# Kernel tuning notes

Hardware: AMD Instinct MI355X
Metric: run time of the kernel (lower is better)

## Reference

```python
import jax, jax.numpy as jnp
import numpy as np

B, T, D = 4, 4096, 768      # batch, tokens, n_embd
S = 1024                    # memory_slots (divides T -> adaptive pool == window mean)
K = 8                       # memory_topk
RW = 0.1                    # memory_retrieval_weight


def setup_inputs() -> dict:
    key = jax.random.key(0)
    ks = jax.random.split(key, 10)
    w = 1.0 / np.sqrt(D).astype(np.float32)
    return {
        "x": jax.random.normal(ks[0], (B, T, D), jnp.float32),
        "Wq": jax.random.normal(ks[1], (D, D), jnp.float32) * w,
        "bq": jnp.zeros((D,), jnp.float32),
        "Wk": jax.random.normal(ks[2], (D, D), jnp.float32) * w,
        "bk": jnp.zeros((D,), jnp.float32),
        "Wv": jax.random.normal(ks[3], (D, D), jnp.float32) * w,
        "bv": jnp.zeros((D,), jnp.float32),
        "Wp": jax.random.normal(ks[4], (D, D), jnp.float32) * w,
        "bp": jnp.zeros((D,), jnp.float32),
        "persistent_memory": jax.random.normal(ks[5], (S, D), jnp.float32),
    }


def reference(x, Wq, bq, Wk, bk, Wv, bv, Wp, bp, persistent_memory):
    # _build_memory_slots: adaptive_avg_pool1d to S slots; T % S == 0 so it is a window mean
    pooled = x.reshape(B, S, T // S, D).mean(axis=2)                    # [B,S,D]
    pers = jnp.broadcast_to(persistent_memory[None], (B, S, D))         # persistent bank
    slots = jnp.concatenate([pooled, pers], axis=1)                     # [B,2S,D]

    q = x @ Wq + bq                                                     # [B,T,D]
    k = slots @ Wk + bk                                                 # [B,2S,D]
    v = slots @ Wv + bv                                                 # [B,2S,D]

    scores = jnp.einsum('btd,bsd->bts', q, k) / jnp.sqrt(jnp.float32(D))  # [B,T,2S]
    top_s, top_i = jax.lax.top_k(scores, K)                             # [B,T,K]
    w = jax.nn.softmax(top_s, axis=-1)                                  # softmax over top-k only

    # gather top-k values: [B,T,K,D]
    vg = jnp.take_along_axis(v, top_i.reshape(B, T * K)[:, :, None], axis=1)
    vg = vg.reshape(B, T, K, D)
    retrieved = jnp.einsum('btk,btkd->btd', w, vg)                      # weighted combine

    return RW * (retrieved @ Wp + bp)                                   # proj * retrieval_weight
```

## Files before the change

### kernel.cpp

```cpp
#include <hip/hip_runtime.h>
#include <math.h>

#define BB 4
#define TT 4096
#define DD 768
#define SS 1024
#define S2 2048
#define KTOP 8
#define RWEIGHT 0.1f
#define TAU 2e-4f
#define AMB_CAP 256

typedef __attribute__((ext_vector_type(8))) _Float16 f16x8;
typedef __attribute__((ext_vector_type(4))) float f32x4;
typedef _Float16 f16;

__device__ __forceinline__ size_t fragoff(int row, int k) {
    return ((size_t)(row >> 4) * 24 + (k >> 5)) * 512 +
           (((row & 15) + (((k >> 3) & 3) << 4)) << 3) + (k & 7);
}

__global__ __launch_bounds__(256) void build_pooled_all(
    const float* __restrict__ x, float* __restrict__ slots)
{
    int i = blockIdx.x * 256 + threadIdx.x;
    int s2 = i / DD;
    int d = i - s2 * DD;
    int b = s2 >> 10, s = s2 & 1023;
    const float* xb = x + (size_t)b * TT * DD + (size_t)(4 * s) * DD + d;
    slots[i] = 0.25f * (xb[0] + xb[DD] + xb[2 * DD] + xb[3 * DD]);
}

__global__ __launch_bounds__(256) void transpose_split(
    const float* __restrict__ W0, const float* __restrict__ W1,
    const float* __restrict__ W2, const float* __restrict__ W3,
    f16* __restrict__ WQh, f16* __restrict__ WQm,
    f16* __restrict__ WKh, f16* __restrict__ WKm,
    f16* __restrict__ WVh, f16* __restrict__ WPh,
    float* __restrict__ WkT32)
{
    const int z = blockIdx.z;
    const float* W = (z == 0) ? W0 : (z == 1) ? W1 : (z == 2) ? W2 : W3;
    __shared__ float t[32][33];
    int bx = blockIdx.x * 32, by = blockIdx.y * 32;
    int lx = threadIdx.x & 31, ly = threadIdx.x >> 5;
#pragma unroll
    for (int r = 0; r < 32; r += 8)
        t[ly + r][lx] = W[(size_t)(bx + ly + r) * 768 + by + lx];
    __syncthreads();
#pragma unroll
    for (int r = 0; r < 32; r += 8) {
        float w = t[lx][ly + r];
        int n = by + ly + r, k = bx + lx;
        size_t fo = fragoff(n, k);
        f16 h = (f16)w;
        if (z == 0) { WQh[fo] = h; WQm[fo] = (f16)(w - (float)h); }
        else if (z == 1) { WKh[fo] = h; WKm[fo] = (f16)(w - (float)h);
                           WkT32[(size_t)n * 768 + k] = w; }
        else if (z == 2) { WVh[fo] = h; }
        else { WPh[fo] = h; }
    }
}

__global__ void zeroN(int* p) { p[threadIdx.x] = 0; }

__device__ __forceinline__ void tile_split_prod(
    const float* __restrict__ A, int arow0,
    const f16* __restrict__ BhF, const f16* __restrict__ BmF, int bncol,
    const float* __restrict__ bias,
    f16* __restrict__ ChF, f16* __restrict__ CmF, int crow0,
    f16* LAh, f16* LAm)
{
    const int tid = threadIdx.x;
    const int lane = tid & 63;
    const int wc = (tid >> 6) & 1;
    const int wr = (tid >> 7) & 1;
    const int srow = tid >> 1, c0 = tid & 1;
    const int p0 = c0 ^ (srow & 3) ^ ((srow >> 2) & 1);
    const int wo0 = srow * 32 + p0 * 8, wo1 = wo0 ^ 16;
    const int csw = (((lane >> 4) ^ (lane & 3) ^ ((lane >> 2) & 1)) * 8);

    f32x4 acc[4][4];
#pragma unroll
    for (int i = 0; i < 4; ++i)
#pragma unroll
        for (int j = 0; j < 4; ++j) acc[i][j] = (f32x4){0.f, 0.f, 0.f, 0.f};

    const float* pa = A + (size_t)(arow0 + srow) * 768 + c0 * 8;
    const int rbB0 = bncol / 16 + wc * 4;

    float4 a0 = *(const float4*)(pa);
    float4 a1 = *(const float4*)(pa + 4);
    float4 a2 = *(const float4*)(pa + 16);
    float4 a3 = *(const float4*)(pa + 20);

    for (int kb = 0; kb < 24; ++kb) {
        __syncthreads();
        {
            float av[16] = {a0.x, a0.y, a0.z, a0.w, a1.x, a1.y, a1.z, a1.w,
                            a2.x, a2.y, a2.z, a2.w, a3.x, a3.y, a3.z, a3.w};
            f16x8 h, m;
#pragma unroll
            for (int j = 0; j < 8; ++j) {
                f16 hh = (f16)av[j]; h[j] = hh; m[j] = (f16)(av[j] - (float)hh);
            }
            *(f16x8*)&LAh[wo0] = h; *(f16x8*)&LAm[wo0] = m;
#pragma unroll
            for (int j = 0; j < 8; ++j) {
                f16 hh = (f16)av[j + 8]; h[j] = hh; m[j] = (f16)(av[j + 8] - (float)hh);
            }
            *(f16x8*)&LAh[wo1] = h; *(f16x8*)&LAm[wo1] = m;
        }
        __syncthreads();

        if (kb + 1 < 24) {
            int k0 = (kb + 1) * 32;
            a0 = *(const float4*)(pa + k0);
            a1 = *(const float4*)(pa + k0 + 4);
            a2 = *(const float4*)(pa + k0 + 16);
            a3 = *(const float4*)(pa + k0 + 20);
        }

        f16x8 fbh[4], fbm[4];
#pragma unroll
        for (int ni = 0; ni < 4; ++ni) {
            size_t off = ((size_t)(rbB0 + ni) * 24 + kb) * 512 + lane * 8;
            fbh[ni] = *(const f16x8*)&BhF[off];
            fbm[ni] = *(const f16x8*)&BmF[off];
        }
        f16x8 fah[4], fam[4];
#pragma unroll
        for (int mi = 0; mi < 4; ++mi) {
            int off = (wr * 64 + mi * 16 + (lane & 15)) * 32 + csw;
            fah[mi] = *(const f16x8*)&LAh[off];
            fam[mi] = *(const f16x8*)&LAm[off];
        }
#pragma unroll
        for (int mi = 0; mi < 4; ++mi)
#pragma unroll
            for (int ni = 0; ni < 4; ++ni) {
                acc[mi][ni] = __builtin_amdgcn_mfma_f32_16x16x32_f16(
                    fah[mi], fbh[ni], acc[mi][ni], 0, 0, 0);
                acc[mi][ni] = __builtin_amdgcn_mfma_f32_16x16x32_f16(
                    fah[mi], fbm[ni], acc[mi][ni], 0, 0, 0);
                acc[mi][ni] = __builtin_amdgcn_mfma_f32_16x16x32_f16(
                    fam[mi], fbh[ni], acc[mi][ni], 0, 0, 0);
            }
    }

    const int orow0 = wr * 64 + (lane >> 4) * 4;
    const int ocol0 = wc * 64 + (lane & 15);
#pragma unroll
    for (int mi = 0; mi < 4; ++mi)
#pragma unroll
        for (int ni = 0; ni < 4; ++ni) {
            int kk = bncol + ocol0 + ni * 16;
            float badd = bias[kk];
            int rbase = crow0 + orow0 + mi * 16;
#pragma unroll
            for (int r = 0; r < 4; ++r) {
                float val = acc[mi][ni][r] + badd;
                f16 h = (f16)val;
                size_t fo = fragoff(rbase + r, kk);
                ChF[fo] = h;
                CmF[fo] = (f16)(val - (float)h);
            }
        }
}

__device__ __forceinline__ void tile_1p_prod(
    const float* __restrict__ A, int arow0,
    const f16* __restrict__ BhF, int bncol,
    const float* __restrict__ bias,
    f16* __restrict__ Co, int crow0, f16* LA)
{
    const int tid = threadIdx.x;
    const int lane = tid & 63;
    const int wc = (tid >> 6) & 1;
    const int wr = (tid >> 7) & 1;
    const int srow = tid >> 1, c0 = tid & 1;
    const int p0 = c0 ^ (srow & 3) ^ ((srow >> 2) & 1);
    const int wo0 = srow * 32 + p0 * 8, wo1 = wo0 ^ 16;
    const int csw = (((lane >> 4) ^ (lane & 3) ^ ((lane >> 2) & 1)) * 8);

    f32x4 acc[4][4];
#pragma unroll
    for (int i = 0; i < 4; ++i)
#pragma unroll
        for (int j = 0; j < 4; ++j) acc[i][j] = (f32x4){0.f, 0.f, 0.f, 0.f};

    const float* pa = A + (size_t)(arow0 + srow) * 768 + c0 * 8;
    const int rbB0 = bncol / 16 + wc * 4;

    float4 a0 = *(const float4*)(pa);
    float4 a1 = *(const float4*)(pa + 4);
    float4 a2 = *(const float4*)(pa + 16);
    float4 a3 = *(const float4*)(pa + 20);

    for (int kb = 0; kb < 24; ++kb) {
        __syncthreads();
        {
            f16x8 h;
            h[0] = (f16)a0.x; h[1] = (f16)a0.y; h[2] = (f16)a0.z; h[3] = (f16)a0.w;
            h[4] = (f16)a1.x; h[5] = (f16)a1.y; h[6] = (f16)a1.z; h[7] = (f16)a1.w;
            *(f16x8*)&LA[wo0] = h;
            h[0] = (f16)a2.x; h[1] = (f16)a2.y; h[2] = (f16)a2.z; h[3] = (f16)a2.w;
            h[4] = (f16)a3.x; h[5] = (f16)a3.y; h[6] = (f16)a3.z; h[7] = (f16)a3.w;
            *(f16x8*)&LA[wo1] = h;
        }
        __syncthreads();

        if (kb + 1 < 24) {
            int k0 = (kb + 1) * 32;
            a0 = *(const float4*)(pa + k0);
            a1 = *(const float4*)(pa + k0 + 4);
            a2 = *(const float4*)(pa + k0 + 16);
            a3 = *(const float4*)(pa + k0 + 20);
        }

        f16x8 fbh[4];
#pragma unroll
        for (int ni = 0; ni < 4; ++ni)
            fbh[ni] = *(const f16x8*)&BhF[((size_t)(rbB0 + ni) * 24 + kb) * 512 + lane * 8];
        f16x8 fah[4];
#pragma unroll
        for (int mi = 0; mi < 4; ++mi)
            fah[mi] = *(const f16x8*)&LA[(wr * 64 + mi * 16 + (lane & 15)) * 32 + csw];
#pragma unroll
        for (int mi = 0; mi < 4; ++mi)
#pragma unroll
            for (int ni = 0; ni < 4; ++ni)
                acc[mi][ni] = __builtin_amdgcn_mfma_f32_16x16x32_f16(
                    fah[mi], fbh[ni], acc[mi][ni], 0, 0, 0);
    }

    const int orow0 = wr * 64 + (lane >> 4) * 4;
    const int ocol0 = wc * 64 + (lane & 15);
#pragma unroll
    for (int mi = 0; mi < 4; ++mi)
#pragma unroll
        for (int ni = 0; ni < 4; ++ni) {
            size_t col = (size_t)bncol + ocol0 + ni * 16;
            float badd = bias[col];
            size_t rbase = (size_t)crow0 + orow0 + mi * 16;
#pragma unroll
            for (int r = 0; r < 4; ++r)
                Co[(rbase + r) * 768 + col] = (f16)(acc[mi][ni][r] + badd);
        }
}

__device__ __forceinline__ void tile_proj_frag(
    const f16* __restrict__ AF, int arow0,
    const f16* __restrict__ BhF, int bncol,
    const float* __restrict__ bias,
    float* __restrict__ Co, int crow0)
{
    const int tid = threadIdx.x;
    const int lane = tid & 63;
    const int wc = (tid >> 6) & 1;
    const int wr = (tid >> 7) & 1;

    f32x4 acc[4][4];
#pragma unroll
    for (int i = 0; i < 4; ++i)
#pragma unroll
        for (int j = 0; j < 4; ++j) acc[i][j] = (f32x4){0.f, 0.f, 0.f, 0.f};

    const int rbA0 = arow0 / 16 + wr * 4;
    const int rbB0 = bncol / 16 + wc * 4;

    for (int kb = 0; kb < 24; ++kb) {
        f16x8 fah[4], fbh[4];
#pragma unroll
        for (int mi = 0; mi < 4; ++mi)
            fah[mi] = *(const f16x8*)&AF[((size_t)(rbA0 + mi) * 24 + kb) * 512 + lane * 8];
#pragma unroll
        for (int ni = 0; ni < 4; ++ni)
            fbh[ni] = *(const f16x8*)&BhF[((size_t)(rbB0 + ni) * 24 + kb) * 512 + lane * 8];
#pragma unroll
        for (int mi = 0; mi < 4; ++mi)
#pragma unroll
            for (int ni = 0; ni < 4; ++ni)
                acc[mi][ni] = __builtin_amdgcn_mfma_f32_16x16x32_f16(
                    fah[mi], fbh[ni], acc[mi][ni], 0, 0, 0);
    }

    const int orow0 = wr * 64 + (lane >> 4) * 4;
    const int ocol0 = wc * 64 + (lane & 15);
#pragma unroll
    for (int mi = 0; mi < 4; ++mi)
#pragma unroll
        for (int ni = 0; ni < 4; ++ni) {
            size_t col = (size_t)bncol + ocol0 + ni * 16;
            float badd = RWEIGHT * bias[col];
            size_t rbase = (size_t)crow0 + orow0 + mi * 16;
#pragma unroll
            for (int r = 0; r < 4; ++r)
                Co[(rbase + r) * 768 + col] = RWEIGHT * acc[mi][ni][r] + badd;
        }
}

__device__ __forceinline__ void tile_scores_frag(
    const f16* __restrict__ qhF, const f16* __restrict__ qmF, int arow0,
    const f16* __restrict__ khF, const f16* __restrict__ kmF, int bncol,
    float* __restrict__ C, float alpha)
{
    const int tid = threadIdx.x;
    const int lane = tid & 63;
    const int wc = (tid >> 6) & 1;
    const int wr = (tid >> 7) & 1;

    f32x4 acc[4][4];
#pragma unroll
    for (int i = 0; i < 4; ++i)
#pragma unroll
        for (int j = 0; j < 4; ++j) acc[i][j] = (f32x4){0.f, 0.f, 0.f, 0.f};

    const int rbA0 = arow0 / 16 + wr * 4;
    const int rbB0 = bncol / 16 + wc * 4;

    for (int kb = 0; kb < 24; ++kb) {
        f16x8 fah[4], fam[4], fbh[4], fbm[4];
#pragma unroll
        for (int mi = 0; mi < 4; ++mi) {
            size_t off = ((size_t)(rbA0 + mi) * 24 + kb) * 512 + lane * 8;
            fah[mi] = *(const f16x8*)&qhF[off];
            fam[mi] = *(const f16x8*)&qmF[off];
        }
#pragma unroll
        for (int ni = 0; ni < 4; ++ni) {
            size_t off = ((size_t)(rbB0 + ni) * 24 + kb) * 512 + lane * 8;
            fbh[ni] = *(const f16x8*)&khF[off];
            fbm[ni] = *(const f16x8*)&kmF[off];
        }
#pragma unroll
        for (int mi = 0; mi < 4; ++mi)
#pragma unroll
            for (int ni = 0; ni < 4; ++ni) {
                acc[mi][ni] = __builtin_amdgcn_mfma_f32_16x16x32_f16(
                    fah[mi], fbh[ni], acc[mi][ni], 0, 0, 0);
                acc[mi][ni] = __builtin_amdgcn_mfma_f32_16x16x32_f16(
                    fah[mi], fbm[ni], acc[mi][ni], 0, 0, 0);
                acc[mi][ni] = __builtin_amdgcn_mfma_f32_16x16x32_f16(
                    fam[mi], fbh[ni], acc[mi][ni], 0, 0, 0);
            }
    }

    const int orow0 = wr * 64 + (lane >> 4) * 4;
    const int ocol0 = wc * 64 + (lane & 15);
#pragma unroll
    for (int mi = 0; mi < 4; ++mi)
#pragma unroll
        for (int ni = 0; ni < 4; ++ni) {
            size_t col = (size_t)bncol + ocol0 + ni * 16;
            size_t rbase = (size_t)arow0 + orow0 + mi * 16;
#pragma unroll
            for (int r = 0; r < 4; ++r)
                C[(rbase + r) * S2 + col] = alpha * acc[mi][ni][r];
        }
}

__global__ __launch_bounds__(256) void megaSelProd(
    int nSel, const float* __restrict__ scores, const f16* __restrict__ v16r,
    f16* __restrict__ retrW, int gbase,
    int* __restrict__ ambc, int* __restrict__ ambgrow, int* __restrict__ cand,
    float* __restrict__ oldw, f16* __restrict__ vsave,
    int hasQ, int hasKV, int doPm,
    const float* __restrict__ xq, const float* __restrict__ slots_b,
    const float* __restrict__ pm,
    const f16* __restrict__ WQh, const f16* __restrict__ WQm,
    const f16* __restrict__ WKh, const f16* __restrict__ WKm,
    const f16* __restrict__ WVh,
    const float* __restrict__ bq, const float* __restrict__ bk,
    const float* __restrict__ bv,
    f16* __restrict__ qh, f16* __restrict__ qm,
    f16* __restrict__ kh, f16* __restrict__ km,
    f16* __restrict__ v16w, f16* __restrict__ v16w2)
{
    __shared__ f16 LAh[4096], LAm[4096];
    int t = blockIdx.x;

    if (hasQ) {
        if (t < 192) {
            tile_split_prod(xq, (t / 6) * 128, WQh, WQm, (t % 6) * 128, bq,
                            qh, qm, (t / 6) * 128, LAh, LAm);
            return;
        }
        t -= 192;
    }
    if (hasKV) {
        if (t < 48) {
            tile_split_prod(slots_b, (t / 6) * 128, WKh, WKm, (t % 6) * 128, bk,
                            kh, km, (t / 6) * 128, LAh, LAm);
            return;
        }
        t -= 48;
        if (doPm) {
            if (t < 48) {
                tile_split_prod(pm, (t / 6) * 128, WKh, WKm, (t % 6) * 128, bk,
                                kh, km, 1024 + (t / 6) * 128, LAh, LAm);
                return;
            }
            t -= 48;
        }
        if (t < 48) {
            tile_1p_prod(slots_b, (t / 6) * 128, WVh, (t % 6) * 128, bv,
                         v16w, (t / 6) * 128, LAh);
            return;
        }
        t -= 48;
        if (doPm) {
            if (t < 48) {
                tile_1p_prod(pm, (t / 6) * 128, WVh, (t % 6) * 128, bv,
                             v16w, 1024 + (t / 6) * 128, LAh);
                return;
            }
            t -= 48;
            if (t < 48) {
                tile_1p_prod(pm, (t / 6) * 128, WVh, (t % 6) * 128, bv,
                             v16w2, 1024 + (t / 6) * 128, LAh);
                return;
            }
            t -= 48;
        }
    }
    if (t >= nSel) return;

    const int lane = threadIdx.x & 63;
    const int wave = threadIdx.x >> 6;
    const int row = t * 4 + wave;
    const float* srow = scores + (size_t)row * S2;
    float vals[32];
#pragma unroll
    for (int i = 0; i < 32; ++i) vals[i] = srow[lane + (i << 6)];

    float topv[16]; int topi[16];
    bool amb = false;
    int nr = 9;
    for (int r = 0; r < 16; ++r) {
        if (r >= nr) break;
        float bvv = -3.4e38f; int bii = 0x7fffffff;
#pragma unroll
        for (int i = 0; i < 32; ++i)
            if (vals[i] > bvv) { bvv = vals[i]; bii = lane + (i << 6); }
#pragma unroll
        for (int off = 32; off > 0; off >>= 1) {
            float ov = __shfl_xor(bvv, off);
            int   oi = __shfl_xor(bii, off);
            if (ov > bvv || (ov == bvv && oi < bii)) { bvv = ov; bii = oi; }
        }
        topv[r] = bvv; topi[r] = bii;
        if ((bii & 63) == lane) vals[bii >> 6] = -3.4e38f;
        if (r == 8) {
            amb = (topv[7] - topv[8]) < TAU;
            if (amb) nr = 16;
        }
    }

    float m = topv[0], w[KTOP], sum = 0.f;
#pragma unroll
    for (int r = 0; r < KTOP; ++r) { w[r] = expf(topv[r] - m); sum += w[r]; }
    float inv = 1.f / sum;
#pragma unroll
    for (int r = 0; r < KTOP; ++r) w[r] *= inv;

    if (amb) {
        int idx = 0;
        if (lane == 0) idx = atomicAdd(ambc, 1);
        idx = __shfl(idx, 0);
        if (idx < AMB_CAP) {
            if (lane == 0) ambgrow[idx] = gbase + row;
            if (lane < 16) cand[idx * 16 + lane] = topi[lane];
            if (lane < KTOP) oldw[idx * KTOP + lane] = w[lane];
            f16* vs = vsave + (size_t)idx * 16 * 768;
            for (int cc = lane; cc < 16 * 96; cc += 64) {
                int cr = cc / 96, ch = cc - cr * 96;
                *(f16x8*)&vs[(size_t)cr * 768 + ch * 8] =
                    *(const f16x8*)&v16r[(size_t)topi[cr] * 768 + ch * 8];
            }
        }
    }

    for (int c = lane; c < 96; c += 64) {
        float o[8] = {0, 0, 0, 0, 0, 0, 0, 0};
#pragma unroll
        for (int r = 0; r < KTOP; ++r) {
            f16x8 vv = *(const f16x8*)&v16r[(size_t)topi[r] * 768 + c * 8];
#pragma unroll
            for (int j = 0; j < 8; ++j) o[j] += w[r] * (float)vv[j];
        }
        f16x8 hx;
#pragma unroll
        for (int j = 0; j < 8; ++j) hx[j] = (f16)o[j];
        size_t fo = ((size_t)(row >> 4) * 24 + (c >> 2)) * 512 +
                    (((row & 15) + ((c & 3) << 4)) << 3);
        *(f16x8*)&retrW[fo] = hx;
    }
}

__global__ __launch_bounds__(256) void megaScoresProj(
    int nSc, const f16* __restrict__ qh, const f16* __restrict__ qm,
    const f16* __restrict__ kh, const f16* __restrict__ km,
    float* __restrict__ scores, float alpha,
    const f16* __restrict__ retrR, const f16* __restrict__ WPh,
    const float* __restrict__ bp, float* __restrict__ outp)
{
    int t = blockIdx.x;
    if (t < nSc) {
        tile_scores_frag(qh, qm, (t >> 4) * 128, kh, km, (t & 15) * 128,
                         scores, alpha);
        return;
    }
    t -= nSc;
    tile_proj_frag(retrR, (t / 6) * 128, WPh, (t % 6) * 128, bp,
                   outp, (t / 6) * 128);
}

__global__ __launch_bounds__(256) void fixA(
    const int* __restrict__ amb_count, const int* __restrict__ amb_grow,
    const float* __restrict__ x, const float* __restrict__ Wq,
    const float* __restrict__ bq, double* __restrict__ q64buf)
{
    int n = *amb_count; if (n > AMB_CAP) n = AMB_CAP;
    const int i = blockIdx.y;
    if (i >= n) return;
    const int tid = threadIdx.x;
    const int jl = tid & 63;
    const int ks = tid >> 6;
    const int j = blockIdx.x * 64 + jl;
    const int grow = amb_grow[i];

    __shared__ float xs[768];
    __shared__ double ps[4][64];
    for (int t = tid; t < 768; t += 256) xs[t] = x[(size_t)grow * 768 + t];
    __syncthreads();

    double a0 = 0.0, a1 = 0.0;
    const float* wp = Wq + j;
    const int k0 = ks * 192;
#pragma unroll 8
    for (int k = 0; k < 192; k += 2) {
        a0 = fma((double)xs[k0 + k],     (double)wp[(size_t)(k0 + k) * 768],     a0);
        a1 = fma((double)xs[k0 + k + 1], (double)wp[(size_t)(k0 + k + 1) * 768], a1);
    }
    ps[ks][jl] = a0 + a1;
    __syncthreads();
    if (ks == 0)
        q64buf[(size_t)i * 768 + j] =
            ((ps[0][jl] + ps[1][jl]) + (ps[2][jl] + ps[3][jl])) + (double)bq[j];
}

__global__ __launch_bounds__(256) void fixB(
    const int* __restrict__ amb_count,
    const float* __restrict__ WkT, const float* __restrict__ bk,
    const double* __restrict__ q64buf,
    double* __restrict__ ubuf, double* __restrict__ bkqbuf)
{
    int n = *amb_count; if (n > AMB_CAP) n = AMB_CAP;
    const int i = blockIdx.y;
    if (i >= n) return;
    const int tid = threadIdx.x;
    const int tl = tid & 63;
    const int js = tid >> 6;
    const int t = blockIdx.x * 64 + tl;

    __shared__ double qs[768];
    __shared__ double ps[4][64];
    const double* qrow = q64buf + (size_t)i * 768;
    for (int k = tid; k < 768; k += 256) qs[k] = qrow[k];
    __syncthreads();

    double a0 = 0.0, a1 = 0.0;
    const float* wp = WkT + t;
    const int j0 = js * 192;
#pragma unroll 8
    for (int k = 0; k < 192; k += 2) {
        a0 = fma((double)wp[(size_t)(j0 + k) * 768],     qs[j0 + k],     a0);
        a1 = fma((double)wp[(size_t)(j0 + k + 1) * 768], qs[j0 + k + 1], a1);
    }
    ps[js][tl] = a0 + a1;
    __syncthreads();
    if (js == 0)
        ubuf[(size_t)i * 768 + t] = (ps[0][tl] + ps[1][tl]) + (ps[2][tl] + ps[3][tl]);

    if (blockIdx.x == 0 && tid < 64) {
        double p = 0.0;
#pragma unroll
        for (int c = 0; c < 12; ++c) {
            int jj = tid + (c << 6);
            p = fma((double)bk[jj], qs[jj], p);
        }
#pragma unroll
        for (int off = 32; off; off >>= 1) p += __shfl_xor(p, off);
        if (tid == 0) bkqbuf[i] = p;
    }
}

__global__ __launch_bounds__(256) void fixC(
    const int* __restrict__ amb_count, const int* __restrict__ amb_grow,
    const float* __restrict__ x, const float* __restrict__ pm,
    const int* __restrict__ cand, const float* __restrict__ oldw,
    const double* __restrict__ ubuf, const double* __restrict__ bkqbuf,
    const f16* __restrict__ vsave, float* __restrict__ dret)
{
    int n = *amb_count; if (n > AMB_CAP) n = AMB_CAP;
    const int i = blockIdx.x;
    if (i >= n) return;
    const int tid = threadIdx.x;
    const int lane = tid & 63;
    const int wave = tid >> 6;
    const int grow = amb_grow[i];
    const float* xb = x + (size_t)(grow >> 12) * TT * 768;

    __shared__ double us[768];
    __shared__ double cs_s[16];
    __shared__ float coef[16];

    const double* urow = ubuf + (size_t)i * 768;
    for (int t = tid; t < 768; t += 256) us[t] = urow[t];
    __syncthreads();

    const double ISQ = 1.0 / sqrt((double)DD);
    const double bkq = bkqbuf[i];
#pragma unroll
    for (int c = wave; c < 16; c += 4) {
        int s = cand[i * 16 + c];
        double p = 0.0;
        if (s < SS) {
            const float* xr = xb + (size_t)(4 * s) * 768;
#pragma unroll
            for (int t = 0; t < 12; ++t) {
                int j2 = lane + (t << 6);
                double sv = 0.25 * ((double)xr[j2] + (double)xr[j2 + 768] +
                                    (double)xr[j2 + 1536] + (double)xr[j2 + 2304]);
                p = fma(sv, us[j2], p);
            }
        } else {
            const float* pr = pm + (size_t)(s - SS) * 768;
#pragma unroll
            for (int t = 0; t < 12; ++t) {
                int j2 = lane + (t << 6);
                p = fma((double)pr[j2], us[j2], p);
            }
        }
#pragma unroll
        for (int off = 32; off; off >>= 1) p += __shfl_xor(p, off);
        if (lane == 0) cs_s[c] = (p + bkq) * ISQ;
    }
    __syncthreads();

    if (tid == 0) {
        double cs[16]; int ci[16];
        for (int c = 0; c < 16; ++c) { cs[c] = cs_s[c]; ci[c] = cand[i * 16 + c]; }
        unsigned used = 0;
        double sv[KTOP]; int sp[KTOP];
        for (int r = 0; r < KTOP; ++r) {
            int bi = -1;
            for (int c = 0; c < 16; ++c) {
                if (used & (1u << c)) continue;
                if (bi < 0 || cs[c] > cs[bi] ||
                    (cs[c] == cs[bi] && ci[c] < ci[bi])) bi = c;
            }
            used |= (1u << bi); sv[r] = cs[bi]; sp[r] = bi;
        }
        double mx = sv[0], es[KTOP], ssum = 0.0;
        for (int r = 0; r < KTOP; ++r) { es[r] = exp(sv[r] - mx); ssum += es[r]; }
        for (int c = 0; c < 16; ++c) coef[c] = (c < KTOP) ? -oldw[i * KTOP + c] : 0.f;
        for (int r = 0; r < KTOP; ++r) coef[sp[r]] += (float)(es[r] / ssum);
    }
    __syncthreads();

    const f16* vs = vsave + (size_t)i * 16 * 768;
    for (int j = tid; j < 768; j += 256) {
        float d = 0.f;
#pragma unroll
        for (int c = 0; c < 16; ++c) d += coef[c] * (float)vs[(size_t)c * 768 + j];
        dret[(size_t)i * 768 + j] = d;
    }
}

__global__ __launch_bounds__(256) void fixD(
    const int* __restrict__ amb_count, const int* __restrict__ amb_grow,
    const float* __restrict__ dret, const float* __restrict__ Wp,
    float* __restrict__ out)
{
    int n = *amb_count; if (n > AMB_CAP) n = AMB_CAP;
    const int i = blockIdx.y;
    if (i >= n) return;
    const int tid = threadIdx.x;
    const int jl = tid & 63;
    const int ks = tid >> 6;
    const int j = blockIdx.x * 64 + jl;
    const int grow = amb_grow[i];

    __shared__ float ds[768];
    __shared__ float ps[4][64];
    for (int t = tid; t < 768; t += 256) ds[t] = dret[(size_t)i * 768 + t];
    __syncthreads();

    float a0 = 0.f, a1 = 0.f;
    const float* wp = Wp + j;
    const int k0 = ks * 192;
#pragma unroll 8
    for (int k = 0; k < 192; k += 2) {
        a0 = fmaf(ds[k0 + k],     wp[(size_t)(k0 + k) * 768],     a0);
        a1 = fmaf(ds[k0 + k + 1], wp[(size_t)(k0 + k + 1) * 768], a1);
    }
    ps[ks][jl] = a0 + a1;
    __syncthreads();
    if (ks == 0)
        out[(size_t)grow * 768 + j] +=
            RWEIGHT * ((ps[0][jl] + ps[1][jl]) + (ps[2][jl] + ps[3][jl]));
}

extern "C" void kernel_launch(void* const* d_in, const int* in_sizes, int n_in,
                              void* d_out, int out_size, void* d_ws, size_t ws_size,
                              hipStream_t stream)
{
    const float* x  = (const float*)d_in[0];
    const float* Wq = (const float*)d_in[1];
    const float* bq = (const float*)d_in[2];
    const float* Wk = (const float*)d_in[3];
    const float* bk = (const float*)d_in[4];
    const float* Wv = (const float*)d_in[5];
    const float* bv = (const float*)d_in[6];
    const float* Wp = (const float*)d_in[7];
    const float* bp = (const float*)d_in[8];
    const float* pm = (const float*)d_in[9];
    float* out = (float*)d_out;
    float* ws  = (float*)d_ws;

    const float inv_sqrt_d = (float)(1.0 / sqrt((double)DD));
    const size_t TD  = (size_t)TT * DD;
    const size_t SD  = (size_t)SS * DD;
    const size_t WSZ = (size_t)DD * DD;

    float* p = ws;
    f16* WQh = (f16*)p; p += WSZ / 2;
    f16* WQm = (f16*)p; p += WSZ / 2;
    f16* WKh = (f16*)p; p += WSZ / 2;
    f16* WKm = (f16*)p; p += WSZ / 2;
    f16* WVh = (f16*)p; p += WSZ / 2;
    f16* WPh = (f16*)p; p += WSZ / 2;
    float* WkT32 = p; p += WSZ;
    float* slots_all = p; p += (size_t)BB * SD;
    f16* qh = (f16*)p; p += TD / 2;
    f16* qm = (f16*)p; p += TD / 2;
    f16* kh = (f16*)p; p += SD;
    f16* km = (f16*)p; p += SD;
    f16* v16a = (f16*)p; p += SD;
    f16* v16b = (f16*)p; p += SD;
    f16* retrA = (f16*)p; p += TD / 2;
    f16* retrB = (f16*)p; p += TD / 2;
    double* q64buf = (double*)p; p += (size_t)AMB_CAP * DD * 2;
    double* ubuf   = (double*)p; p += (size_t)AMB_CAP * DD * 2;
    double* bkqbuf = (double*)p; p += AMB_CAP * 2;
    int* cand = (int*)p; p += (size_t)AMB_CAP * 16;
    float* oldw = p; p += (size_t)AMB_CAP * KTOP;
    f16* vsave = (f16*)p; p += (size_t)AMB_CAP * 16 * DD / 2;
    float* dret = p; p += (size_t)AMB_CAP * DD;
    int* ambc = (int*)p; p += 64;
    int* ambgrow = (int*)p; p += AMB_CAP;
    float* scores = p;

    transpose_split<<<dim3(24, 24, 4), 256, 0, stream>>>(
        Wq, Wk, Wv, Wp, WQh, WQm, WKh, WKm, WVh, WPh, WkT32);
    zeroN<<<1, 64, 0, stream>>>(ambc);
    build_pooled_all<<<(BB * SS * DD) / 256, 256, 0, stream>>>(x, slots_all);

    megaSelProd<<<432, 256, 0, stream>>>(
        0, nullptr, nullptr, nullptr, 0, ambc, ambgrow, cand, oldw, vsave,
        1, 1, 1, x, slots_all, pm,
        WQh, WQm, WKh, WKm, WVh, bq, bk, bv, qh, qm, kh, km, v16a, v16b);
    megaScoresProj<<<512, 256, 0, stream>>>(
        512, qh, qm, kh, km, scores, inv_sqrt_d, nullptr, WPh, bp, nullptr);

    for (int b = 1; b < BB; ++b) {
        f16* v16w = (b & 1) ? v16b : v16a;
        f16* v16r = ((b - 1) & 1) ? v16b : v16a;
        f16* retrW = ((b - 1) & 1) ? retrB : retrA;

        megaSelProd<<<1312, 256, 0, stream>>>(
            1024, scores, v16r, retrW, (b - 1) * TT,
            ambc, ambgrow, cand, oldw, vsave,
            1, 1, 0, x + (size_t)b * TD, slots_all + (size_t)b * SD, nullptr,
            WQh, WQm, WKh, WKm, WVh, bq, bk, bv, qh, qm, kh, km, v16w, nullptr);
        megaScoresProj<<<704, 256, 0, stream>>>(
            512, qh, qm, kh, km, scores, inv_sqrt_d,
            retrW, WPh, bp, out + (size_t)(b - 1) * TD);
    }

    f16* v16r3 = v16b;
    f16* retrW3 = retrB;
    megaSelProd<<<1024, 256, 0, stream>>>(
        1024, scores, v16r3, retrW3, 3 * TT,
        ambc, ambgrow, cand, oldw, vsave,
        0, 0, 0, nullptr, nullptr, nullptr,
        WQh, WQm, WKh, WKm, WVh, bq, bk, bv, qh, qm, kh, km, nullptr, nullptr);
    megaScoresProj<<<192, 256, 0, stream>>>(
        0, nullptr, nullptr, nullptr, nullptr, nullptr, 0.f,
        retrW3, WPh, bp, out + (size_t)3 * TD);

    fixA<<<dim3(12, AMB_CAP), 256, 0, stream>>>(ambc, ambgrow, x, Wq, bq, q64buf);
    fixB<<<dim3(12, AMB_CAP), 256, 0, stream>>>(ambc, WkT32, bk, q64buf, ubuf, bkqbuf);
    fixC<<<AMB_CAP, 256, 0, stream>>>(ambc, ambgrow, x, pm, cand, oldw,
                                      ubuf, bkqbuf, vsave, dret);
    fixD<<<dim3(12, AMB_CAP), 256, 0, stream>>>(ambc, ambgrow, dret, Wp, out);
}
```

Measured before the change: 663.9 us.

## Store q/k/retrieved as row-major planes and stage through swizzled LDS

Intermediate q, k and retrieved tensors are now written row-major instead of in the pre-swizzled MFMA fragment layout. The scores and projection tiles load them with coalesced global reads into XOR-swizzled shared memory, prefetching the next k-slice into registers. The aim is cheaper, more coalesced epilogue stores in the producers. The cost is extra LDS traffic, two barriers per k-step, and 32 KB of shared memory per block in the scores/proj kernel, which may lower occupancy.

```diff
diff --git a/kernel.cpp b/kernel.cpp
--- a/kernel.cpp
+++ b/kernel.cpp
@@ -68,7 +68,7 @@
     const float* __restrict__ A, int arow0,
     const f16* __restrict__ BhF, const f16* __restrict__ BmF, int bncol,
     const float* __restrict__ bias,
-    f16* __restrict__ ChF, f16* __restrict__ CmF, int crow0,
+    f16* __restrict__ Ch, f16* __restrict__ Cm, int crow0,
     f16* LAh, f16* LAm)
 {
     const int tid = threadIdx.x;
@@ -154,16 +154,16 @@
     for (int mi = 0; mi < 4; ++mi)
 #pragma unroll
         for (int ni = 0; ni < 4; ++ni) {
-            int kk = bncol + ocol0 + ni * 16;
-            float badd = bias[kk];
-            int rbase = crow0 + orow0 + mi * 16;
+            size_t col = (size_t)bncol + ocol0 + ni * 16;
+            float badd = bias[col];
+            size_t rbase = (size_t)crow0 + orow0 + mi * 16;
 #pragma unroll
             for (int r = 0; r < 4; ++r) {
                 float val = acc[mi][ni][r] + badd;
                 f16 h = (f16)val;
-                size_t fo = fragoff(rbase + r, kk);
-                ChF[fo] = h;
-                CmF[fo] = (f16)(val - (float)h);
+                size_t idx = (rbase + r) * 768 + col;
+                Ch[idx] = h;
+                Cm[idx] = (f16)(val - (float)h);
             }
         }
 }
@@ -249,16 +249,20 @@
         }
 }
 
-__device__ __forceinline__ void tile_proj_frag(
-    const f16* __restrict__ AF, int arow0,
+__device__ __forceinline__ void tile_proj(
+    const f16* __restrict__ A, int arow0,
     const f16* __restrict__ BhF, int bncol,
     const float* __restrict__ bias,
-    float* __restrict__ Co, int crow0)
+    float* __restrict__ Co, int crow0, f16* LA)
 {
     const int tid = threadIdx.x;
     const int lane = tid & 63;
     const int wc = (tid >> 6) & 1;
     const int wr = (tid >> 7) & 1;
+    const int srow = tid >> 1, c0 = tid & 1;
+    const int p0 = c0 ^ (srow & 3) ^ ((srow >> 2) & 1);
+    const int wo0 = srow * 32 + p0 * 8, wo1 = wo0 ^ 16;
+    const int csw = (((lane >> 4) ^ (lane & 3) ^ ((lane >> 2) & 1)) * 8);
 
     f32x4 acc[4][4];
 #pragma unroll
@@ -266,17 +270,32 @@
 #pragma unroll
         for (int j = 0; j < 4; ++j) acc[i][j] = (f32x4){0.f, 0.f, 0.f, 0.f};
 
-    const int rbA0 = arow0 / 16 + wr * 4;
+    const f16* pa = A + (size_t)(arow0 + srow) * 768 + c0 * 8;
     const int rbB0 = bncol / 16 + wc * 4;
 
+    f16x8 ah0 = *(const f16x8*)(pa);
+    f16x8 ah1 = *(const f16x8*)(pa + 16);
+
     for (int kb = 0; kb < 24; ++kb) {
-        f16x8 fah[4], fbh[4];
-#pragma unroll
-        for (int mi = 0; mi < 4; ++mi)
-            fah[mi] = *(const f16x8*)&AF[((size_t)(rbA0 + mi) * 24 + kb) * 512 + lane * 8];
+        __syncthreads();
+        *(f16x8*)&LA[wo0] = ah0;
+        *(f16x8*)&LA[wo1] = ah1;
+        __syncthreads();
+
+        if (kb + 1 < 24) {
+            int k0 = (kb + 1) * 32;
+            ah0 = *(const f16x8*)(pa + k0);
+            ah1 = *(const f16x8*)(pa + k0 + 16);
+        }
+
+        f16x8 fbh[4];
 #pragma unroll
         for (int ni = 0; ni < 4; ++ni)
             fbh[ni] = *(const f16x8*)&BhF[((size_t)(rbB0 + ni) * 24 + kb) * 512 + lane * 8];
+        f16x8 fah[4];
+#pragma unroll
+        for (int mi = 0; mi < 4; ++mi)
+            fah[mi] = *(const f16x8*)&LA[(wr * 64 + mi * 16 + (lane & 15)) * 32 + csw];
 #pragma unroll
         for (int mi = 0; mi < 4; ++mi)
 #pragma unroll
@@ -300,15 +319,21 @@
         }
 }
 
-__device__ __forceinline__ void tile_scores_frag(
-    const f16* __restrict__ qhF, const f16* __restrict__ qmF, int arow0,
-    const f16* __restrict__ khF, const f16* __restrict__ kmF, int bncol,
-    float* __restrict__ C, float alpha)
+__device__ __forceinline__ void tile_scores_planes(
+    const f16* __restrict__ qh, const f16* __restrict__ qm, int arow0,
+    const f16* __restrict__ kh, const f16* __restrict__ km, int bncol,
+    float* __restrict__ C, float alpha,
+    f16* LAh, f16* LAm, f16* LBh, f16* LBm)
 {
     const int tid = threadIdx.x;
     const int lane = tid & 63;
     const int wc = (tid >> 6) & 1;
     const int wr = (tid >> 7) & 1;
+    const int srow = tid >> 1, c0 = tid & 1;
+    const int p0 = c0 ^ (srow & 3) ^ ((srow >> 2) & 1);
+    const int wo0 = srow * 32 + p0 * 8, wo1 = wo0 ^ 16;
+    const int csw = (((lane >> 4) ^ (lane & 3) ^ ((lane >> 2) & 1)) * 8);
+    const size_t bn = (size_t)bncol;
 
     f32x4 acc[4][4];
 #pragma unroll
@@ -316,22 +341,51 @@
 #pragma unroll
         for (int j = 0; j < 4; ++j) acc[i][j] = (f32x4){0.f, 0.f, 0.f, 0.f};
 
-    const int rbA0 = arow0 / 16 + wr * 4;
-    const int rbB0 = bncol / 16 + wc * 4;
-
-    for (int kb = 0; kb < 24; ++kb) {
+    const f16* pah = qh + (size_t)(arow0 + srow) * 768 + c0 * 8;
+    const f16* pam = qm + (size_t)(arow0 + srow) * 768 + c0 * 8;
+    const f16* pbh = kh + (bn + srow) * 768 + c0 * 8;
+    const f16* pbm = km + (bn + srow) * 768 + c0 * 8;
+
+    f16x8 ah0 = *(const f16x8*)(pah);
+    f16x8 ah1 = *(const f16x8*)(pah + 16);
+    f16x8 am0 = *(const f16x8*)(pam);
+    f16x8 am1 = *(const f16x8*)(pam + 16);
+    f16x8 bh0 = *(const f16x8*)(pbh);
+    f16x8 bh1 = *(const f16x8*)(pbh + 16);
+    f16x8 bm0 = *(const f16x8*)(pbm);
+    f16x8 bm1 = *(const f16x8*)(pbm + 16);
+
+    for (int k0 = 0; k0 < 768; k0 += 32) {
+        __syncthreads();
+        *(f16x8*)&LAh[wo0] = ah0; *(f16x8*)&LAh[wo1] = ah1;
+        *(f16x8*)&LAm[wo0] = am0; *(f16x8*)&LAm[wo1] = am1;
+        *(f16x8*)&LBh[wo0] = bh0; *(f16x8*)&LBh[wo1] = bh1;
+        *(f16x8*)&LBm[wo0] = bm0; *(f16x8*)&LBm[wo1] = bm1;
+        __syncthreads();
+
+        if (k0 + 32 < 768) {
+            ah0 = *(const f16x8*)(pah + k0 + 32);
+            ah1 = *(const f16x8*)(pah + k0 + 48);
+            am0 = *(const f16x8*)(pam + k0 + 32);
+            am1 = *(const f16x8*)(pam + k0 + 48);
+            bh0 = *(const f16x8*)(pbh + k0 + 32);
+            bh1 = *(const f16x8*)(pbh + k0 + 48);
+            bm0 = *(const f16x8*)(pbm + k0 + 32);
+            bm1 = *(const f16x8*)(pbm + k0 + 48);
+        }
+
         f16x8 fah[4], fam[4], fbh[4], fbm[4];
 #pragma unroll
         for (int mi = 0; mi < 4; ++mi) {
-            size_t off = ((size_t)(rbA0 + mi) * 24 + kb) * 512 + lane * 8;
-            fah[mi] = *(const f16x8*)&qhF[off];
-            fam[mi] = *(const f16x8*)&qmF[off];
+            int off = (wr * 64 + mi * 16 + (lane & 15)) * 32 + csw;
+            fah[mi] = *(const f16x8*)&LAh[off];
+            fam[mi] = *(const f16x8*)&LAm[off];
         }
 #pragma unroll
         for (int ni = 0; ni < 4; ++ni) {
-            size_t off = ((size_t)(rbB0 + ni) * 24 + kb) * 512 + lane * 8;
-            fbh[ni] = *(const f16x8*)&khF[off];
-            fbm[ni] = *(const f16x8*)&kmF[off];
+            int off = (wc * 64 + ni * 16 + (lane & 15)) * 32 + csw;
+            fbh[ni] = *(const f16x8*)&LBh[off];
+            fbm[ni] = *(const f16x8*)&LBm[off];
         }
 #pragma unroll
         for (int mi = 0; mi < 4; ++mi)
@@ -352,7 +406,7 @@
     for (int mi = 0; mi < 4; ++mi)
 #pragma unroll
         for (int ni = 0; ni < 4; ++ni) {
-            size_t col = (size_t)bncol + ocol0 + ni * 16;
+            size_t col = bn + ocol0 + ni * 16;
             size_t rbase = (size_t)arow0 + orow0 + mi * 16;
 #pragma unroll
             for (int r = 0; r < 4; ++r)
@@ -492,9 +546,7 @@
         f16x8 hx;
 #pragma unroll
         for (int j = 0; j < 8; ++j) hx[j] = (f16)o[j];
-        size_t fo = ((size_t)(row >> 4) * 24 + (c >> 2)) * 512 +
-                    (((row & 15) + ((c & 3) << 4)) << 3);
-        *(f16x8*)&retrW[fo] = hx;
+        *(f16x8*)&retrW[(size_t)row * 768 + c * 8] = hx;
     }
 }
 
@@ -505,15 +557,16 @@
     const f16* __restrict__ retrR, const f16* __restrict__ WPh,
     const float* __restrict__ bp, float* __restrict__ outp)
 {
+    __shared__ f16 LAh[4096], LAm[4096], LBh[4096], LBm[4096];
     int t = blockIdx.x;
     if (t < nSc) {
-        tile_scores_frag(qh, qm, (t >> 4) * 128, kh, km, (t & 15) * 128,
-                         scores, alpha);
+        tile_scores_planes(qh, qm, (t >> 4) * 128, kh, km, (t & 15) * 128,
+                           scores, alpha, LAh, LAm, LBh, LBm);
         return;
     }
     t -= nSc;
-    tile_proj_frag(retrR, (t / 6) * 128, WPh, (t % 6) * 128, bp,
-                   outp, (t / 6) * 128);
+    tile_proj(retrR, (t / 6) * 128, WPh, (t % 6) * 128, bp,
+              outp, (t / 6) * 128, LAh);
 }
 
 __global__ __launch_bounds__(256) void fixA(
```

Result: faster. 621.1 us (-6.4%).
